# Performance work log

Measured on AMD Instinct MI355X. Metric: run time of the kernel, lower is better.

## Reference

```python
import jax, jax.numpy as jnp
import numpy as np


def setup_inputs() -> dict:
    key = jax.random.key(0)
    k1, k2 = jax.random.split(key)
    T, D, E = 8192, 4096, 64
    x = jax.random.normal(k1, (T, D), dtype=jnp.float32)
    gate_w = jax.random.normal(k2, (E, D), dtype=jnp.float32) * (1.0 / np.sqrt(D))
    return {"x": x, "gate_w": gate_w}


def reference(x, gate_w):
    TOPK = 8
    # logits = x @ W^T, computed in float32 like .float() in torch
    logits = jnp.einsum('td,ed->te', x, gate_w).astype(jnp.float32)
    scores = jax.nn.sigmoid(scores_in := logits) if False else jax.nn.sigmoid(logits)
    # top-k scores per token; values are exactly the gathered weights
    weights, indices = jax.lax.top_k(scores, TOPK)
    weights = weights / jnp.clip(jnp.sum(weights, axis=-1, keepdims=True), 1e-12)
    return weights.astype(x.dtype), indices
```

## Files before the change

kernel.cpp:

```cpp
#include <hip/hip_runtime.h>
#include <math.h>

#define T_TOTAL 8192
#define D_TOTAL 4096
#define E 64
#define TOPK 8
#define NKB (D_TOTAL / 32)

#define WVS 8
#define WKCH (D_TOTAL / WVS)
#define TOKB 32

typedef short short8 __attribute__((ext_vector_type(8)));
typedef float f32x4 __attribute__((ext_vector_type(4)));

__device__ __forceinline__ void split3(const float* v8, short8& h, short8& m, short8& l) {
#pragma unroll
    for (int j = 0; j < 8; ++j) {
        const float f = v8[j];
        const unsigned u = __float_as_uint(f);
        const unsigned hu = u & 0xffff0000u;
        const float r1 = f - __uint_as_float(hu);
        const unsigned mu = __float_as_uint(r1) & 0xffff0000u;
        const float r2 = r1 - __uint_as_float(mu);
        const unsigned lu = __float_as_uint(r2);
        h[j] = (short)(hu >> 16);
        m[j] = (short)(mu >> 16);
        l[j] = (short)(lu >> 16);
    }
}

__device__ __forceinline__ void split3v(const float* v, short8& h, short8& m, short8& l) {
    unsigned* hp = reinterpret_cast<unsigned*>(&h);
    unsigned* mp = reinterpret_cast<unsigned*>(&m);
    unsigned* lp = reinterpret_cast<unsigned*>(&l);
#pragma unroll
    for (int p = 0; p < 4; ++p) {
        const float a = v[2 * p], b = v[2 * p + 1];
        const unsigned hw = __builtin_amdgcn_perm(__float_as_uint(b), __float_as_uint(a), 0x07060302u);
        const float r0 = a - __uint_as_float(hw << 16);
        const float r1 = b - __uint_as_float(hw & 0xffff0000u);
        const unsigned mw = __builtin_amdgcn_perm(__float_as_uint(r1), __float_as_uint(r0), 0x07060302u);
        const float s0 = r0 - __uint_as_float(mw << 16);
        const float s1 = r1 - __uint_as_float(mw & 0xffff0000u);
        const unsigned lw = __builtin_amdgcn_perm(__float_as_uint(s1), __float_as_uint(s0), 0x07060302u);
        hp[p] = hw; mp[p] = mw; lp[p] = lw;
    }
}

__global__ __launch_bounds__(256)
void prep_w(const float* __restrict__ w, short8* __restrict__ Bh,
            short8* __restrict__ Bm, short8* __restrict__ Bl) {
    const int t = blockIdx.x * 256 + threadIdx.x;
    const int lane = t & 63;
    const int nt = (t >> 6) & 3;
    const int kb = t >> 8;
    const int e = nt * 16 + (lane & 15);
    const int k = kb * 32 + (lane >> 4) * 8;

    const float* src = w + (size_t)e * D_TOTAL + k;
    float v[8];
    *reinterpret_cast<float4*>(&v[0]) = *reinterpret_cast<const float4*>(src);
    *reinterpret_cast<float4*>(&v[4]) = *reinterpret_cast<const float4*>(src + 4);

    short8 h, m, l;
    split3(v, h, m, l);
    Bh[t] = h; Bm[t] = m; Bl[t] = l;
}

__global__ __launch_bounds__(512, 4)
void fused_router(const float* __restrict__ x,
                  const short8* __restrict__ Bh, const short8* __restrict__ Bm,
                  const short8* __restrict__ Bl,
                  float* __restrict__ out) {
    __shared__ float tiles[4][2048];
    __shared__ float fin[2048];

    const int tid = threadIdx.x;
    const int lane = tid & 63;
    const int wv = tid >> 6;
    const int tok0 = blockIdx.x * TOKB;

    const int row = lane & 15;
    const int kq = lane >> 4;
    const float* xb = x + (size_t)(tok0 + row) * D_TOTAL + wv * WKCH + kq * 8;

    f32x4 acc[2][4];
#pragma unroll
    for (int m = 0; m < 2; ++m)
#pragma unroll
        for (int n = 0; n < 4; ++n) acc[m][n] = (f32x4){0.f, 0.f, 0.f, 0.f};

    float xr[2][2][8];
#pragma unroll
    for (int m = 0; m < 2; ++m) {
        const float* ap = xb + (size_t)(m * 16) * D_TOTAL;
        *reinterpret_cast<float4*>(&xr[0][m][0]) = *reinterpret_cast<const float4*>(ap);
        *reinterpret_cast<float4*>(&xr[0][m][4]) = *reinterpret_cast<const float4*>(ap + 4);
    }

#pragma unroll
    for (int kb = 0; kb < 16; ++kb) {
        const int gkb = wv * 16 + kb;

        short8 bh[4], bm_[4], bl[4];
#pragma unroll
        for (int nt = 0; nt < 4; ++nt) {
            const size_t bi = (size_t)(gkb * 4 + nt) * 64 + lane;
            bh[nt]  = Bh[bi];
            bm_[nt] = Bm[bi];
            bl[nt]  = Bl[bi];
        }

        if (kb < 15) {
#pragma unroll
            for (int m = 0; m < 2; ++m) {
                const float* ap = xb + (size_t)(m * 16) * D_TOTAL + (kb + 1) * 32;
                *reinterpret_cast<float4*>(&xr[(kb + 1) & 1][m][0]) = *reinterpret_cast<const float4*>(ap);
                *reinterpret_cast<float4*>(&xr[(kb + 1) & 1][m][4]) = *reinterpret_cast<const float4*>(ap + 4);
            }
        }

#pragma unroll
        for (int m = 0; m < 2; ++m) {
            short8 ah, am_, al;
            split3v(xr[kb & 1][m], ah, am_, al);
#pragma unroll
            for (int nt = 0; nt < 4; ++nt) acc[m][nt] = __builtin_amdgcn_mfma_f32_16x16x32_bf16(ah,  bh[nt],  acc[m][nt], 0, 0, 0);
#pragma unroll
            for (int nt = 0; nt < 4; ++nt) acc[m][nt] = __builtin_amdgcn_mfma_f32_16x16x32_bf16(ah,  bm_[nt], acc[m][nt], 0, 0, 0);
#pragma unroll
            for (int nt = 0; nt < 4; ++nt) acc[m][nt] = __builtin_amdgcn_mfma_f32_16x16x32_bf16(am_, bh[nt],  acc[m][nt], 0, 0, 0);
#pragma unroll
            for (int nt = 0; nt < 4; ++nt) acc[m][nt] = __builtin_amdgcn_mfma_f32_16x16x32_bf16(am_, bm_[nt], acc[m][nt], 0, 0, 0);
#pragma unroll
            for (int nt = 0; nt < 4; ++nt) acc[m][nt] = __builtin_amdgcn_mfma_f32_16x16x32_bf16(ah,  bl[nt],  acc[m][nt], 0, 0, 0);
#pragma unroll
            for (int nt = 0; nt < 4; ++nt) acc[m][nt] = __builtin_amdgcn_mfma_f32_16x16x32_bf16(al,  bh[nt],  acc[m][nt], 0, 0, 0);
        }
    }

    if (wv >= 4) {
        float* s = &tiles[wv - 4][lane];
#pragma unroll
        for (int m = 0; m < 2; ++m)
#pragma unroll
            for (int nt = 0; nt < 4; ++nt)
#pragma unroll
                for (int r = 0; r < 4; ++r)
                    s[(m * 16 + nt * 4 + r) * 64] = acc[m][nt][r];
    }
    __syncthreads();
    if (wv < 4) {
        float* s = &tiles[wv][lane];
#pragma unroll
        for (int m = 0; m < 2; ++m)
#pragma unroll
            for (int nt = 0; nt < 4; ++nt)
#pragma unroll
                for (int r = 0; r < 4; ++r) {
                    const int j = (m * 16 + nt * 4 + r) * 64;
                    s[j] = acc[m][nt][r] + s[j];
                }
    }
    __syncthreads();

#pragma unroll
    for (int p = 0; p < 4; ++p) {
        const int j4 = tid + p * 512;
        float s0 = tiles[0][j4] + tiles[1][j4];
        s0 += tiles[2][j4] + tiles[3][j4];
        const int j = j4 >> 6, ln = j4 & 63;
        const int t = (j >> 4) * 16 + (ln >> 4) * 4 + (j & 3);
        const int e = ((j >> 2) & 3) * 16 + (ln & 15);
        fin[t * 64 + e] = s0;
    }
    __syncthreads();

#pragma unroll
    for (int rep = 0; rep < 4; ++rep) {
        const int t = wv * 4 + rep;
        float v = fin[t * 64 + lane];
        float wj[TOPK];
        int   ij[TOPK];
        float wsum = 0.f;
#pragma unroll
        for (int j = 0; j < TOPK; ++j) {
            float mx = v;
#pragma unroll
            for (int off = 32; off >= 1; off >>= 1)
                mx = fmaxf(mx, __shfl_xor(mx, off));
            const unsigned long long msk = __ballot(v == mx);
            const int widx = (int)__builtin_ctzll(msk);
            wj[j] = 1.f / (1.f + expf(-mx));
            ij[j] = widx;
            wsum += wj[j];
            if (lane == widx) v = -INFINITY;
        }
        const float inv = 1.f / fmaxf(wsum, 1e-12f);
        const int tg = tok0 + t;
        if (lane == 0) {
#pragma unroll
            for (int j = 0; j < TOPK; ++j)
                out[(size_t)tg * TOPK + j] = wj[j] * inv;
#pragma unroll
            for (int j = 0; j < TOPK; ++j)
                out[(size_t)T_TOTAL * TOPK + (size_t)tg * TOPK + j] = (float)ij[j];
        }
    }
}

extern "C" void kernel_launch(void* const* d_in, const int* in_sizes, int n_in,
                              void* d_out, int out_size, void* d_ws, size_t ws_size,
                              hipStream_t stream) {
    const float* x = (const float*)d_in[0];
    const float* w = (const float*)d_in[1];
    float* out = (float*)d_out;

    short8* Bh = (short8*)d_ws;
    short8* Bm = Bh + (size_t)NKB * 4 * 64;
    short8* Bl = Bm + (size_t)NKB * 4 * 64;

    prep_w<<<NKB * 4 * 64 / 256, 256, 0, stream>>>(w, Bh, Bm, Bl);
    fused_router<<<T_TOTAL / TOKB, 512, 0, stream>>>(x, Bh, Bm, Bl, out);
}
```

Baseline: 53.36 us.

## Split K across 16 waves per block and reorder prefetch before B loads

Doubles the block to 1024 threads so each of 16 waves handles a 256-wide K slice instead of 512, halving per-wave serial MFMA work for the same 32 tokens. The cross-wave reduction now sums eight LDS tiles, and each thread writes two output entries. The x prefetch is moved ahead of the B loads, with compiler barriers to keep that order. Costs are more LDS (about 72KB per block), a larger reduction, and possibly lower occupancy.

```diff
diff --git a/kernel.cpp b/kernel.cpp
--- a/kernel.cpp
+++ b/kernel.cpp
@@ -6,10 +6,6 @@
 #define E 64
 #define TOPK 8
 #define NKB (D_TOTAL / 32)
-
-#define WVS 8
-#define WKCH (D_TOTAL / WVS)
-#define TOKB 32
 
 typedef short short8 __attribute__((ext_vector_type(8)));
 typedef float f32x4 __attribute__((ext_vector_type(4)));
@@ -68,22 +64,22 @@
     Bh[t] = h; Bm[t] = m; Bl[t] = l;
 }
 
-__global__ __launch_bounds__(512, 4)
+__global__ __launch_bounds__(1024, 4)
 void fused_router(const float* __restrict__ x,
                   const short8* __restrict__ Bh, const short8* __restrict__ Bm,
                   const short8* __restrict__ Bl,
                   float* __restrict__ out) {
-    __shared__ float tiles[4][2048];
+    __shared__ float tiles[8 * 2048];
     __shared__ float fin[2048];
 
     const int tid = threadIdx.x;
     const int lane = tid & 63;
     const int wv = tid >> 6;
-    const int tok0 = blockIdx.x * TOKB;
+    const int tok0 = blockIdx.x * 32;
 
     const int row = lane & 15;
     const int kq = lane >> 4;
-    const float* xb = x + (size_t)(tok0 + row) * D_TOTAL + wv * WKCH + kq * 8;
+    const float* xb = x + (size_t)(tok0 + row) * D_TOTAL + wv * 256 + kq * 8;
 
     f32x4 acc[2][4];
 #pragma unroll
@@ -91,17 +87,28 @@
 #pragma unroll
         for (int n = 0; n < 4; ++n) acc[m][n] = (f32x4){0.f, 0.f, 0.f, 0.f};
 
-    float xr[2][2][8];
+    float xbuf[2][2][8];
 #pragma unroll
     for (int m = 0; m < 2; ++m) {
         const float* ap = xb + (size_t)(m * 16) * D_TOTAL;
-        *reinterpret_cast<float4*>(&xr[0][m][0]) = *reinterpret_cast<const float4*>(ap);
-        *reinterpret_cast<float4*>(&xr[0][m][4]) = *reinterpret_cast<const float4*>(ap + 4);
-    }
-
-#pragma unroll
-    for (int kb = 0; kb < 16; ++kb) {
-        const int gkb = wv * 16 + kb;
+        *reinterpret_cast<float4*>(&xbuf[0][m][0]) = *reinterpret_cast<const float4*>(ap);
+        *reinterpret_cast<float4*>(&xbuf[0][m][4]) = *reinterpret_cast<const float4*>(ap + 4);
+    }
+    asm volatile("" ::: "memory");
+
+#pragma unroll
+    for (int kb = 0; kb < 8; ++kb) {
+        const int gkb = wv * 8 + kb;
+
+        if (kb < 7) {
+#pragma unroll
+            for (int m = 0; m < 2; ++m) {
+                const float* ap = xb + (size_t)(m * 16) * D_TOTAL + (kb + 1) * 32;
+                *reinterpret_cast<float4*>(&xbuf[(kb + 1) & 1][m][0]) = *reinterpret_cast<const float4*>(ap);
+                *reinterpret_cast<float4*>(&xbuf[(kb + 1) & 1][m][4]) = *reinterpret_cast<const float4*>(ap + 4);
+            }
+        }
+        asm volatile("" ::: "memory");
 
         short8 bh[4], bm_[4], bl[4];
 #pragma unroll
@@ -111,20 +118,12 @@
             bm_[nt] = Bm[bi];
             bl[nt]  = Bl[bi];
         }
-
-        if (kb < 15) {
-#pragma unroll
-            for (int m = 0; m < 2; ++m) {
-                const float* ap = xb + (size_t)(m * 16) * D_TOTAL + (kb + 1) * 32;
-                *reinterpret_cast<float4*>(&xr[(kb + 1) & 1][m][0]) = *reinterpret_cast<const float4*>(ap);
-                *reinterpret_cast<float4*>(&xr[(kb + 1) & 1][m][4]) = *reinterpret_cast<const float4*>(ap + 4);
-            }
-        }
+        asm volatile("" ::: "memory");
 
 #pragma unroll
         for (int m = 0; m < 2; ++m) {
             short8 ah, am_, al;
-            split3v(xr[kb & 1][m], ah, am_, al);
+            split3v(xbuf[kb & 1][m], ah, am_, al);
 #pragma unroll
             for (int nt = 0; nt < 4; ++nt) acc[m][nt] = __builtin_amdgcn_mfma_f32_16x16x32_bf16(ah,  bh[nt],  acc[m][nt], 0, 0, 0);
 #pragma unroll
@@ -140,8 +139,8 @@
         }
     }
 
-    if (wv >= 4) {
-        float* s = &tiles[wv - 4][lane];
+    if (wv >= 8) {
+        float* s = &tiles[(size_t)(wv - 8) * 2048 + lane];
 #pragma unroll
         for (int m = 0; m < 2; ++m)
 #pragma unroll
@@ -151,8 +150,8 @@
                     s[(m * 16 + nt * 4 + r) * 64] = acc[m][nt][r];
     }
     __syncthreads();
-    if (wv < 4) {
-        float* s = &tiles[wv][lane];
+    if (wv < 8) {
+        float* s = &tiles[(size_t)wv * 2048 + lane];
 #pragma unroll
         for (int m = 0; m < 2; ++m)
 #pragma unroll
@@ -165,21 +164,24 @@
     }
     __syncthreads();
 
-#pragma unroll
-    for (int p = 0; p < 4; ++p) {
-        const int j4 = tid + p * 512;
-        float s0 = tiles[0][j4] + tiles[1][j4];
-        s0 += tiles[2][j4] + tiles[3][j4];
-        const int j = j4 >> 6, ln = j4 & 63;
-        const int t = (j >> 4) * 16 + (ln >> 4) * 4 + (j & 3);
+    {
+        float s0 = 0.f, s1 = 0.f;
+#pragma unroll
+        for (int w2 = 0; w2 < 8; ++w2) {
+            s0 += tiles[w2 * 2048 + tid];
+            s1 += tiles[w2 * 2048 + 1024 + tid];
+        }
+        const int j = tid >> 6, ln = tid & 63;
+        const int t = (ln >> 4) * 4 + (j & 3);
         const int e = ((j >> 2) & 3) * 16 + (ln & 15);
         fin[t * 64 + e] = s0;
+        fin[(t + 16) * 64 + e] = s1;
     }
     __syncthreads();
 
 #pragma unroll
-    for (int rep = 0; rep < 4; ++rep) {
-        const int t = wv * 4 + rep;
+    for (int rep = 0; rep < 2; ++rep) {
+        const int t = wv * 2 + rep;
         float v = fin[t * 64 + lane];
         float wj[TOPK];
         int   ij[TOPK];
@@ -222,5 +224,5 @@
     short8* Bl = Bm + (size_t)NKB * 4 * 64;
 
     prep_w<<<NKB * 4 * 64 / 256, 256, 0, stream>>>(w, Bh, Bm, Bl);
-    fused_router<<<T_TOTAL / TOKB, 512, 0, stream>>>(x, Bh, Bm, Bl, out);
-}
+    fused_router<<<T_TOTAL / 32, 1024, 0, stream>>>(x, Bh, Bm, Bl, out);
+}
```

New measurement: 58.61 us. 9.8% more time.
